# Optimization experiments

Hardware: AMD Instinct MI355X
Metric: run time of the kernel (lower is better)

The kernel has to match this reference:

```python
import jax, jax.numpy as jnp
import numpy as np

N = 16384          # num nodes
D_IN, D_HID, D_OUT = 512, 256, 64
S = 4096           # sampled nodes per layer


def setup_inputs() -> dict:
    key = jax.random.key(0)
    ks = jax.random.split(key, 8)
    X = jax.random.normal(ks[0], (N, D_IN), dtype=jnp.float32)
    A_hat = jax.random.uniform(ks[1], (N, N), dtype=jnp.float32)
    W1 = jax.random.normal(ks[2], (D_IN, D_HID), dtype=jnp.float32) * 0.05
    b1 = jax.random.normal(ks[3], (D_HID,), dtype=jnp.float32) * 0.05
    W2 = jax.random.normal(ks[4], (D_HID, D_OUT), dtype=jnp.float32) * 0.05
    b2 = jax.random.normal(ks[5], (D_OUT,), dtype=jnp.float32) * 0.05
    # unique sampled node ids per layer (avoids nondeterministic duplicate scatter)
    sampled_l0 = jax.random.permutation(ks[6], N)[:S].astype(jnp.int32)
    sampled_l1 = jax.random.permutation(ks[7], N)[:S].astype(jnp.int32)
    return {"X": X, "A_hat": A_hat, "W1": W1, "b1": b1, "W2": W2, "b2": b2,
            "sampled_l0": sampled_l0, "sampled_l1": sampled_l1}


def reference(X, A_hat, W1, b1, W2, b2, sampled_l0, sampled_l1):
    n = X.shape[0]
    s0 = sampled_l0.shape[0]
    s1 = sampled_l1.shape[0]

    # ---- layer 0: sampled = l0, next_sampled = l1 ----
    H_l = jax.nn.relu(X[sampled_l0] @ W1 + b1)                 # [S, D_HID]
    # weights[i,j] = A_hat[next[i], sampled[j]] * N / S  (sampling_probs=None path)
    w0 = A_hat[sampled_l1][:, sampled_l0] * (n / s0)           # [S, S]
    agg0 = w0 @ H_l                                            # [S, D_HID]
    H = jnp.zeros((n, W1.shape[1]), dtype=X.dtype).at[sampled_l1].set(agg0)
    H = jax.nn.relu(H)                                         # inter-layer relu

    # ---- layer 1 (last): sampled = l1, next_sampled = arange(N) ----
    H_l2 = jax.nn.relu(H[sampled_l1] @ W2 + b2)                # [S, D_OUT]
    w1 = A_hat[:, sampled_l1] * (n / s1)                       # [N, S]
    out = w1 @ H_l2                                            # [N, D_OUT]; scatter to arange(N) == identity
    return out
```

## Files before the change

kernel.cpp:

```cpp
#include <hip/hip_runtime.h>
#include <hip/hip_bf16.h>
#include <stdint.h>

typedef __attribute__((ext_vector_type(8))) short short8;
typedef __attribute__((ext_vector_type(4))) float f32x4;

#define N_NODES 16384
#define D_IN    512
#define D_HID   256
#define D_OUT   64
#define S_SAMP  4096

__device__ __forceinline__ unsigned short f2bf(float f) {
  __hip_bfloat16 h = __float2bfloat16(f);
  union { __hip_bfloat16 h; unsigned short u; } cv; cv.h = h; return cv.u;
}

template<int BM, int BN, int BK, bool RELU_A>
__global__ __launch_bounds__(256)
void gemm_tn(const float* __restrict__ A, int lda,
             const int* __restrict__ arow,
             const unsigned short* __restrict__ Bt, int ldb,
             float* __restrict__ C, int ldc,
             int K, int kChunks, float scale)
{
  static_assert(BM == 64 && BK == 64 && (BN == 64 || BN == 256), "tile");
  constexpr int CH    = BK / 8;
  constexpr int RPS   = 512 / BK;
  constexpr int SLABS = BN / RPS;
  constexpr int SLABW = SLABS / 4;

  const int nMt = gridDim.x / kChunks;
  const int mt  = blockIdx.x % nMt;
  const int kc  = blockIdx.x / nMt;
  const int kLen = K / kChunks;
  const int k0   = kc * kLen;
  const int tid  = threadIdx.x;
  const int lane = tid & 63;
  const int wid  = tid >> 6;
  const int l16  = lane & 15;
  const int lg   = lane >> 4;

  __shared__ unsigned short As[BM * BK];
  __shared__ unsigned short Bs[BN * BK];

  constexpr int WN  = (BN == 256) ? 4 : 2;
  constexpr int WM  = 4 / WN;
  constexpr int WTM = BM / WM;
  constexpr int WTN = BN / WN;
  constexpr int MF  = WTM / 16;
  constexpr int NF  = WTN / 16;
  const int wrow = wid / WN;
  const int wcol = wid % WN;

  f32x4 acc[MF][NF] = {};

  const int am   = tid >> 2;
  const int aseg = tid & 3;
  const int arowIdx = mt * BM + am;
  const size_t rowg = arow ? (size_t)arow[arowIdx] : (size_t)arowIdx;
  const float* aBase = A + rowg * (size_t)lda + k0 + aseg * 16;

  const int brow = lane / CH;
  const int bcol = 8 * ((lane % CH) ^ (brow & (CH - 1)));
  const unsigned short* bSrc = Bt + (size_t)brow * ldb + k0 + bcol;

  for (int ks = 0; ks < kLen; ks += BK) {
    __syncthreads();
    #pragma unroll
    for (int i = 0; i < SLABW; ++i) {
      const int s = wid * SLABW + i;
      __builtin_amdgcn_global_load_lds(
          (const __attribute__((address_space(1))) uint32_t*)(bSrc + (size_t)s * RPS * ldb + ks),
          (__attribute__((address_space(3))) uint32_t*)(&Bs[s * 512]),
          16, 0, 0);
    }
    {
      const float* ap = aBase + ks;
      f32x4 v0 = *(const f32x4*)(ap + 0);
      f32x4 v1 = *(const f32x4*)(ap + 4);
      f32x4 v2 = *(const f32x4*)(ap + 8);
      f32x4 v3 = *(const f32x4*)(ap + 12);
      if (RELU_A) {
        #pragma unroll
        for (int j = 0; j < 4; ++j) {
          v0[j] = fmaxf(v0[j], 0.f); v1[j] = fmaxf(v1[j], 0.f);
          v2[j] = fmaxf(v2[j], 0.f); v3[j] = fmaxf(v3[j], 0.f);
        }
      }
      short8 s0, s1;
      s0[0]=f2bf(v0[0]); s0[1]=f2bf(v0[1]); s0[2]=f2bf(v0[2]); s0[3]=f2bf(v0[3]);
      s0[4]=f2bf(v1[0]); s0[5]=f2bf(v1[1]); s0[6]=f2bf(v1[2]); s0[7]=f2bf(v1[3]);
      s1[0]=f2bf(v2[0]); s1[1]=f2bf(v2[1]); s1[2]=f2bf(v2[2]); s1[3]=f2bf(v2[3]);
      s1[4]=f2bf(v3[0]); s1[5]=f2bf(v3[1]); s1[6]=f2bf(v3[2]); s1[7]=f2bf(v3[3]);
      const int g0 = (aseg * 2)     ^ (am & 7);
      const int g1 = (aseg * 2 + 1) ^ (am & 7);
      *(short8*)&As[am * BK + g0 * 8] = s0;
      *(short8*)&As[am * BK + g1 * 8] = s1;
    }
    __syncthreads();
    #pragma unroll
    for (int kk = 0; kk < BK / 32; ++kk) {
      const int gk = kk * 4 + lg;
      short8 af[MF], bfr[NF];
      #pragma unroll
      for (int fm = 0; fm < MF; ++fm) {
        const int m = wrow * WTM + fm * 16 + l16;
        af[fm] = *(const short8*)&As[m * BK + ((gk ^ (m & 7)) * 8)];
      }
      #pragma unroll
      for (int fn = 0; fn < NF; ++fn) {
        const int n = wcol * WTN + fn * 16 + l16;
        bfr[fn] = *(const short8*)&Bs[n * BK + ((gk ^ (n & 7)) * 8)];
      }
      #pragma unroll
      for (int fm = 0; fm < MF; ++fm)
        #pragma unroll
        for (int fn = 0; fn < NF; ++fn)
          acc[fm][fn] = __builtin_amdgcn_mfma_f32_16x16x32_bf16(
              af[fm], bfr[fn], acc[fm][fn], 0, 0, 0);
    }
  }
  #pragma unroll
  for (int fm = 0; fm < MF; ++fm)
    #pragma unroll
    for (int fn = 0; fn < NF; ++fn)
      #pragma unroll
      for (int j = 0; j < 4; ++j) {
        const int r = mt * BM + wrow * WTM + fm * 16 + lg * 4 + j;
        const int c = wcol * WTN + fn * 16 + l16;
        atomicAdd(&C[(size_t)r * ldc + c], scale * acc[fm][fn][j]);
      }
}

__global__ void conv_w_t(const float* __restrict__ W1, const float* __restrict__ W2,
                         unsigned short* __restrict__ W1t, unsigned short* __restrict__ W2t) {
  const int idx = blockIdx.x * 256 + threadIdx.x;
  if (idx < D_IN * D_HID) {
    const int j = idx / D_IN, i = idx % D_IN;
    W1t[idx] = f2bf(W1[(size_t)i * D_HID + j]);
  }
  if (idx < D_HID * D_OUT) {
    const int j = idx / D_HID, i = idx % D_HID;
    W2t[idx] = f2bf(W2[(size_t)i * D_OUT + j]);
  }
}

__global__ void ep_scatter_t(const float* __restrict__ G, const float* __restrict__ bias,
                             const int* __restrict__ rows, unsigned short* __restrict__ BextT,
                             int ncol, int total) {
  const int idx = blockIdx.x * 256 + threadIdx.x;
  if (idx >= total) return;
  const int c = idx / S_SAMP;
  const int r = idx & (S_SAMP - 1);
  float v = G[(size_t)r * ncol + c] + bias[c];
  v = v > 0.f ? v : 0.f;
  BextT[(size_t)c * N_NODES + rows[r]] = f2bf(v);
}

extern "C" void kernel_launch(void* const* d_in, const int* in_sizes, int n_in,
                              void* d_out, int out_size, void* d_ws, size_t ws_size,
                              hipStream_t stream) {
  const float* X     = (const float*)d_in[0];
  const float* A_hat = (const float*)d_in[1];
  const float* W1    = (const float*)d_in[2];
  const float* b1    = (const float*)d_in[3];
  const float* W2    = (const float*)d_in[4];
  const float* b2    = (const float*)d_in[5];
  const int*   l0    = (const int*)d_in[6];
  const int*   l1    = (const int*)d_in[7];
  float* out = (float*)d_out;

  if (ws_size < (size_t)(20u << 20)) return;
  char* ws = (char*)d_ws;
  unsigned short* HextT = (unsigned short*)(ws);
  unsigned short* PextT = (unsigned short*)(ws + (8  << 20));
  float* G1 = (float*)(ws + (10 << 20));
  float* G2 = (float*)(ws + (14 << 20));
  float* G3 = (float*)(ws + (18 << 20));
  unsigned short* W1t = (unsigned short*)(ws + (19 << 20));
  unsigned short* W2t = (unsigned short*)(ws + (19 << 20) + (256 << 10));

  hipMemsetAsync(ws,  0, (size_t)(19u << 20), stream);
  hipMemsetAsync(out, 0, (size_t)N_NODES * D_OUT * 4, stream);

  conv_w_t<<<512, 256, 0, stream>>>(W1, W2, W1t, W2t);

  gemm_tn<64, 256, 64, false><<<(S_SAMP / 64) * 8, 256, 0, stream>>>(
      X, D_IN, l0, W1t, D_IN, G1, D_HID, D_IN, 8, 1.0f);
  ep_scatter_t<<<(S_SAMP * D_HID + 255) / 256, 256, 0, stream>>>(
      G1, b1, l0, HextT, D_HID, S_SAMP * D_HID);

  gemm_tn<64, 256, 64, false><<<(S_SAMP / 64) * 16, 256, 0, stream>>>(
      A_hat, N_NODES, l1, HextT, N_NODES, G2, D_HID, N_NODES, 16, 4.0f);

  gemm_tn<64, 64, 64, true><<<(S_SAMP / 64) * 4, 256, 0, stream>>>(
      G2, D_HID, nullptr, W2t, D_HID, G3, D_OUT, D_HID, 4, 1.0f);
  ep_scatter_t<<<(S_SAMP * D_OUT + 255) / 256, 256, 0, stream>>>(
      G3, b2, l1, PextT, D_OUT, S_SAMP * D_OUT);

  gemm_tn<64, 64, 64, false><<<(N_NODES / 64) * 8, 256, 0, stream>>>(
      A_hat, N_NODES, nullptr, PextT, N_NODES, out, D_OUT, N_NODES, 8, 4.0f);
}
```

Baseline: 383.5 us.

## Fuse epilogues into split-K GEMMs via last-block completion counters

Removes the separate epilogue scatter kernels and the small W2 GEMM. Each split-K GEMM now uses a per-tile atomic counter, and the last finishing block applies bias+ReLU and the scatter; in layer 0 it also runs the H·W2 MFMA product inline. This cuts launches and the round trips of intermediates through global memory. Split-K factors are halved (8→4 and 16→8), the block index mapping is changed, and occupancy hints are added. The cost is a serialized tail on the last block per tile, which adds fences and atomics.

```diff
diff --git a/kernel.cpp b/kernel.cpp
--- a/kernel.cpp
+++ b/kernel.cpp
@@ -16,13 +16,16 @@
   union { __hip_bfloat16 h; unsigned short u; } cv; cv.h = h; return cv.u;
 }
 
-template<int BM, int BN, int BK, bool RELU_A>
-__global__ __launch_bounds__(256)
+template<int BM, int BN, int BK, bool RELU_A, int FIN>
+__global__ __launch_bounds__(256, FIN ? 4 : 1)
 void gemm_tn(const float* __restrict__ A, int lda,
              const int* __restrict__ arow,
              const unsigned short* __restrict__ Bt, int ldb,
              float* __restrict__ C, int ldc,
-             int K, int kChunks, float scale)
+             int K, int kChunks, float scale,
+             const float* __restrict__ bias, const int* __restrict__ rows,
+             unsigned short* __restrict__ dstT, const unsigned short* __restrict__ W2t,
+             int* __restrict__ cnt)
 {
   static_assert(BM == 64 && BK == 64 && (BN == 64 || BN == 256), "tile");
   constexpr int CH    = BK / 8;
@@ -30,9 +33,8 @@
   constexpr int SLABS = BN / RPS;
   constexpr int SLABW = SLABS / 4;
 
-  const int nMt = gridDim.x / kChunks;
-  const int mt  = blockIdx.x % nMt;
-  const int kc  = blockIdx.x / nMt;
+  const int mt  = blockIdx.x / kChunks;
+  const int kc  = blockIdx.x % kChunks;
   const int kLen = K / kChunks;
   const int k0   = kc * kLen;
   const int tid  = threadIdx.x;
@@ -43,6 +45,7 @@
 
   __shared__ unsigned short As[BM * BK];
   __shared__ unsigned short Bs[BN * BK];
+  __shared__ int s_done;
 
   constexpr int WN  = (BN == 256) ? 4 : 2;
   constexpr int WM  = 4 / WN;
@@ -131,6 +134,57 @@
         const int c = wcol * WTN + fn * 16 + l16;
         atomicAdd(&C[(size_t)r * ldc + c], scale * acc[fm][fn][j]);
       }
+
+  if (FIN == 0) return;
+
+  __threadfence();
+  __syncthreads();
+  if (tid == 0) s_done = (atomicAdd(cnt + mt, 1) == kChunks - 1) ? 1 : 0;
+  __syncthreads();
+  if (!s_done) return;
+  __threadfence();
+
+  if (FIN == 1) {
+    const float* Gt = C + (size_t)(mt * BM) * ldc;
+    #pragma unroll 4
+    for (int rr = 0; rr < BM; ++rr) {
+      float v = __hip_atomic_load(&Gt[rr * ldc + tid], __ATOMIC_RELAXED,
+                                  __HIP_MEMORY_SCOPE_AGENT);
+      v = fmaxf(v + bias[tid], 0.f);
+      dstT[(size_t)tid * N_NODES + rows[mt * BM + rr]] = f2bf(v);
+    }
+  } else {
+    const int row = mt * BM + wid * 16 + l16;
+    const float* g2row = C + (size_t)row * ldc;
+    f32x4 acc2[4] = {};
+    #pragma unroll
+    for (int ksf = 0; ksf < D_HID / 32; ++ksf) {
+      const int kb = ksf * 32 + lg * 8;
+      short8 af;
+      #pragma unroll
+      for (int e = 0; e < 8; ++e) {
+        float v = __hip_atomic_load(&g2row[kb + e], __ATOMIC_RELAXED,
+                                    __HIP_MEMORY_SCOPE_AGENT);
+        af[e] = f2bf(fmaxf(v, 0.f));
+      }
+      #pragma unroll
+      for (int fn = 0; fn < 4; ++fn) {
+        short8 bf = *(const short8*)&W2t[(size_t)(fn * 16 + l16) * D_HID + kb];
+        acc2[fn] = __builtin_amdgcn_mfma_f32_16x16x32_bf16(af, bf, acc2[fn], 0, 0, 0);
+      }
+    }
+    #pragma unroll
+    for (int fn = 0; fn < 4; ++fn) {
+      const int c = fn * 16 + l16;
+      const float bv = bias[c];
+      #pragma unroll
+      for (int j = 0; j < 4; ++j) {
+        const int rrow = mt * BM + wid * 16 + lg * 4 + j;
+        float v = fmaxf(acc2[fn][j] + bv, 0.f);
+        dstT[(size_t)c * N_NODES + rows[rrow]] = f2bf(v);
+      }
+    }
+  }
 }
 
 __global__ void conv_w_t(const float* __restrict__ W1, const float* __restrict__ W2,
@@ -144,18 +198,6 @@
     const int j = idx / D_HID, i = idx % D_HID;
     W2t[idx] = f2bf(W2[(size_t)i * D_OUT + j]);
   }
-}
-
-__global__ void ep_scatter_t(const float* __restrict__ G, const float* __restrict__ bias,
-                             const int* __restrict__ rows, unsigned short* __restrict__ BextT,
-                             int ncol, int total) {
-  const int idx = blockIdx.x * 256 + threadIdx.x;
-  if (idx >= total) return;
-  const int c = idx / S_SAMP;
-  const int r = idx & (S_SAMP - 1);
-  float v = G[(size_t)r * ncol + c] + bias[c];
-  v = v > 0.f ? v : 0.f;
-  BextT[(size_t)c * N_NODES + rows[r]] = f2bf(v);
 }
 
 extern "C" void kernel_launch(void* const* d_in, const int* in_sizes, int n_in,
@@ -177,28 +219,25 @@
   unsigned short* PextT = (unsigned short*)(ws + (8  << 20));
   float* G1 = (float*)(ws + (10 << 20));
   float* G2 = (float*)(ws + (14 << 20));
-  float* G3 = (float*)(ws + (18 << 20));
+  int*   cnt1 = (int*)(ws + (18 << 20));
+  int*   cnt2 = cnt1 + 64;
   unsigned short* W1t = (unsigned short*)(ws + (19 << 20));
   unsigned short* W2t = (unsigned short*)(ws + (19 << 20) + (256 << 10));
 
-  hipMemsetAsync(ws,  0, (size_t)(19u << 20), stream);
+  hipMemsetAsync(ws,  0, (size_t)(18u << 20) + 4096, stream);
   hipMemsetAsync(out, 0, (size_t)N_NODES * D_OUT * 4, stream);
 
   conv_w_t<<<512, 256, 0, stream>>>(W1, W2, W1t, W2t);
 
-  gemm_tn<64, 256, 64, false><<<(S_SAMP / 64) * 8, 256, 0, stream>>>(
-      X, D_IN, l0, W1t, D_IN, G1, D_HID, D_IN, 8, 1.0f);
-  ep_scatter_t<<<(S_SAMP * D_HID + 255) / 256, 256, 0, stream>>>(
-      G1, b1, l0, HextT, D_HID, S_SAMP * D_HID);
-
-  gemm_tn<64, 256, 64, false><<<(S_SAMP / 64) * 16, 256, 0, stream>>>(
-      A_hat, N_NODES, l1, HextT, N_NODES, G2, D_HID, N_NODES, 16, 4.0f);
-
-  gemm_tn<64, 64, 64, true><<<(S_SAMP / 64) * 4, 256, 0, stream>>>(
-      G2, D_HID, nullptr, W2t, D_HID, G3, D_OUT, D_HID, 4, 1.0f);
-  ep_scatter_t<<<(S_SAMP * D_OUT + 255) / 256, 256, 0, stream>>>(
-      G3, b2, l1, PextT, D_OUT, S_SAMP * D_OUT);
-
-  gemm_tn<64, 64, 64, false><<<(N_NODES / 64) * 8, 256, 0, stream>>>(
-      A_hat, N_NODES, nullptr, PextT, N_NODES, out, D_OUT, N_NODES, 8, 4.0f);
-}
+  gemm_tn<64, 256, 64, false, 1><<<(S_SAMP / 64) * 4, 256, 0, stream>>>(
+      X, D_IN, l0, W1t, D_IN, G1, D_HID, D_IN, 4, 1.0f,
+      b1, l0, HextT, nullptr, cnt1);
+
+  gemm_tn<64, 256, 64, false, 2><<<(S_SAMP / 64) * 8, 256, 0, stream>>>(
+      A_hat, N_NODES, l1, HextT, N_NODES, G2, D_HID, N_NODES, 8, 4.0f,
+      b2, l1, PextT, W2t, cnt2);
+
+  gemm_tn<64, 64, 64, false, 0><<<(N_NODES / 64) * 8, 256, 0, stream>>>(
+      A_hat, N_NODES, nullptr, PextT, N_NODES, out, D_OUT, N_NODES, 8, 4.0f,
+      nullptr, nullptr, nullptr, nullptr, nullptr);
+}
```

After: 483.9 us. 26.2% more time.

## Replace final A_hat GEMM with LDS-free direct-load MFMA kernel, adjust split-K

Applied to the files above, without the earlier changes.

Adds an LDS-free GEMM kernel for the large N x N by 64 aggregation. Each wave streams its A_hat rows straight from global memory into registers, converts them to bf16 and feeds MFMA, with no shared-memory staging or barriers. The block order is changed so the split-K chunks of one row tile run next to each other, and the split-K factor is halved for the first two GEMMs to cut atomic traffic. The risks are uncoalesced, strided B loads from global memory and lower latency hiding without LDS double buffering.

```diff
diff --git a/kernel.cpp b/kernel.cpp
--- a/kernel.cpp
+++ b/kernel.cpp
@@ -30,9 +30,8 @@
   constexpr int SLABS = BN / RPS;
   constexpr int SLABW = SLABS / 4;
 
-  const int nMt = gridDim.x / kChunks;
-  const int mt  = blockIdx.x % nMt;
-  const int kc  = blockIdx.x / nMt;
+  const int mt  = blockIdx.x / kChunks;
+  const int kc  = blockIdx.x % kChunks;
   const int kLen = K / kChunks;
   const int k0   = kc * kLen;
   const int tid  = threadIdx.x;
@@ -133,6 +132,58 @@
       }
 }
 
+__global__ __launch_bounds__(256, 6)
+void gemm4_direct(const float* __restrict__ A, int lda,
+                  const unsigned short* __restrict__ Bt, int ldb,
+                  float* __restrict__ C, int ldc,
+                  int K, int kChunks, float scale)
+{
+  const int mt   = blockIdx.x / kChunks;
+  const int kc   = blockIdx.x % kChunks;
+  const int kLen = K / kChunks;
+  const int k0   = kc * kLen;
+  const int tid  = threadIdx.x;
+  const int lane = tid & 63;
+  const int wid  = tid >> 6;
+  const int l16  = lane & 15;
+  const int lg   = lane >> 4;
+
+  const int row = mt * 64 + wid * 16 + l16;
+  const float* aPtr = A + (size_t)row * lda + k0 + lg * 8;
+  const unsigned short* bPtr = Bt + (size_t)l16 * ldb + k0 + lg * 8;
+
+  f32x4 acc[4] = {};
+
+  const int nk = kLen / 32;
+  #pragma unroll 4
+  for (int t = 0; t < nk; ++t) {
+    const float* ap = aPtr + t * 32;
+    f32x4 a0 = *(const f32x4*)(ap);
+    f32x4 a1 = *(const f32x4*)(ap + 4);
+    const unsigned short* bp = bPtr + t * 32;
+    short8 b0 = *(const short8*)(bp);
+    short8 b1 = *(const short8*)(bp + (size_t)16 * ldb);
+    short8 b2 = *(const short8*)(bp + (size_t)32 * ldb);
+    short8 b3 = *(const short8*)(bp + (size_t)48 * ldb);
+    short8 af;
+    af[0]=f2bf(a0[0]); af[1]=f2bf(a0[1]); af[2]=f2bf(a0[2]); af[3]=f2bf(a0[3]);
+    af[4]=f2bf(a1[0]); af[5]=f2bf(a1[1]); af[6]=f2bf(a1[2]); af[7]=f2bf(a1[3]);
+    acc[0] = __builtin_amdgcn_mfma_f32_16x16x32_bf16(af, b0, acc[0], 0, 0, 0);
+    acc[1] = __builtin_amdgcn_mfma_f32_16x16x32_bf16(af, b1, acc[1], 0, 0, 0);
+    acc[2] = __builtin_amdgcn_mfma_f32_16x16x32_bf16(af, b2, acc[2], 0, 0, 0);
+    acc[3] = __builtin_amdgcn_mfma_f32_16x16x32_bf16(af, b3, acc[3], 0, 0, 0);
+  }
+
+  #pragma unroll
+  for (int fn = 0; fn < 4; ++fn)
+    #pragma unroll
+    for (int j = 0; j < 4; ++j) {
+      const int rr = mt * 64 + wid * 16 + lg * 4 + j;
+      const int cc = fn * 16 + l16;
+      atomicAdd(&C[(size_t)rr * ldc + cc], scale * acc[fn][j]);
+    }
+}
+
 __global__ void conv_w_t(const float* __restrict__ W1, const float* __restrict__ W2,
                          unsigned short* __restrict__ W1t, unsigned short* __restrict__ W2t) {
   const int idx = blockIdx.x * 256 + threadIdx.x;
@@ -186,19 +237,19 @@
 
   conv_w_t<<<512, 256, 0, stream>>>(W1, W2, W1t, W2t);
 
-  gemm_tn<64, 256, 64, false><<<(S_SAMP / 64) * 8, 256, 0, stream>>>(
-      X, D_IN, l0, W1t, D_IN, G1, D_HID, D_IN, 8, 1.0f);
+  gemm_tn<64, 256, 64, false><<<(S_SAMP / 64) * 4, 256, 0, stream>>>(
+      X, D_IN, l0, W1t, D_IN, G1, D_HID, D_IN, 4, 1.0f);
   ep_scatter_t<<<(S_SAMP * D_HID + 255) / 256, 256, 0, stream>>>(
       G1, b1, l0, HextT, D_HID, S_SAMP * D_HID);
 
-  gemm_tn<64, 256, 64, false><<<(S_SAMP / 64) * 16, 256, 0, stream>>>(
-      A_hat, N_NODES, l1, HextT, N_NODES, G2, D_HID, N_NODES, 16, 4.0f);
+  gemm_tn<64, 256, 64, false><<<(S_SAMP / 64) * 8, 256, 0, stream>>>(
+      A_hat, N_NODES, l1, HextT, N_NODES, G2, D_HID, N_NODES, 8, 4.0f);
 
   gemm_tn<64, 64, 64, true><<<(S_SAMP / 64) * 4, 256, 0, stream>>>(
       G2, D_HID, nullptr, W2t, D_HID, G3, D_OUT, D_HID, 4, 1.0f);
   ep_scatter_t<<<(S_SAMP * D_OUT + 255) / 256, 256, 0, stream>>>(
       G3, b2, l1, PextT, D_OUT, S_SAMP * D_OUT);
 
-  gemm_tn<64, 64, 64, false><<<(N_NODES / 64) * 8, 256, 0, stream>>>(
-      A_hat, N_NODES, nullptr, PextT, N_NODES, out, D_OUT, N_NODES, 8, 4.0f);
-}
+  gemm4_direct<<<(N_NODES / 64) * 8, 256, 0, stream>>>(
+      A_hat, N_NODES, PextT, N_NODES, out, D_OUT, N_NODES, 8, 4.0f);
+}
```

Result: slower. 527.1 us (+37.4%).
